# Optimization experiments

Measured on AMD Instinct MI355X. Metric: run time of the kernel, lower is better.

## Reference

```python
import jax, jax.numpy as jnp
import numpy as np

B, F, H, T = 2048, 128, 512, 96  # batch, n_features, hidden_size, output_length


def setup_inputs() -> dict:
    key = jax.random.key(0)
    ks = jax.random.split(key, 7)
    s_ih = 1.0 / np.sqrt(H)
    return {
        "hidden": jax.random.normal(ks[0], (B, H), dtype=jnp.float32),
        "w_ih": jax.random.uniform(ks[1], (3 * H, F), jnp.float32, -s_ih, s_ih),
        "w_hh": jax.random.uniform(ks[2], (3 * H, H), jnp.float32, -s_ih, s_ih),
        "b_ih": jax.random.uniform(ks[3], (3 * H,), jnp.float32, -s_ih, s_ih),
        "b_hh": jax.random.uniform(ks[4], (3 * H,), jnp.float32, -s_ih, s_ih),
        "fc_w": jax.random.uniform(ks[5], (F, H), jnp.float32, -s_ih, s_ih),
        "fc_b": jax.random.uniform(ks[6], (F,), jnp.float32, -s_ih, s_ih),
    }


def reference(hidden, w_ih, w_hh, b_ih, b_hh, fc_w, fc_b):
    x0 = jnp.zeros((hidden.shape[0], F), dtype=hidden.dtype)  # initial_input=None

    def step(carry, _):
        h, x = carry
        gi = x @ w_ih.T + b_ih            # [B, 3H]
        gh = h @ w_hh.T + b_hh            # [B, 3H]
        i_r, i_z, i_n = jnp.split(gi, 3, axis=-1)
        h_r, h_z, h_n = jnp.split(gh, 3, axis=-1)
        r = jax.nn.sigmoid(i_r + h_r)
        z = jax.nn.sigmoid(i_z + h_z)
        n = jnp.tanh(i_n + r * h_n)
        h_new = (1.0 - z) * n + z * h
        x_new = h_new @ fc_w.T + fc_b     # [B, F]
        return (h_new, x_new), x_new

    _, ys = jax.lax.scan(step, (hidden, x0), None, length=T)  # [T, B, F]
    out = jnp.transpose(ys, (1, 0, 2))     # [B, T, F]
    out = out[:, ::-1, :]                  # backwards=True: outputs.insert(0, ...)
    return out
```

## Files before the change

kernel.cpp:

```cpp
#include <hip/hip_runtime.h>
#include <hip/hip_bf16.h>

#define HH 512
#define FF 128
#define BB 2048
#define TT 96
#define NSTEP 96
#define NGATE 2048
#define NTOT 2176
#define GRP 16
#define CPB 32

typedef short short8 __attribute__((ext_vector_type(8)));
typedef float f32x4 __attribute__((ext_vector_type(4)));

__device__ __forceinline__ float sigmoidf_(float x) { return 1.f / (1.f + __expf(-x)); }
__device__ __forceinline__ float tanhf_(float x) {
    float e = __expf(-2.f * fabsf(x));
    float t = (1.f - e) / (1.f + e);
    return x < 0.f ? -t : t;
}

__device__ __forceinline__ size_t frag_off(int m, int k, int K) {
    return (size_t)((m >> 4) * (K >> 5) + (k >> 5)) * 1024
         + (size_t)(((k >> 3) & 3) * 256 + (m & 15) * 16 + (k & 7) * 2);
}

__device__ __forceinline__ short bf16bits(float f) {
    __hip_bfloat16 b = __float2bfloat16(f);
    return *(short*)&b;
}

__global__ __launch_bounds__(256) void build_weights(
    const float* __restrict__ w_ih, const float* __restrict__ w_hh,
    const float* __restrict__ b_ih, const float* __restrict__ b_hh,
    const float* __restrict__ fc_w, const float* __restrict__ fc_b,
    char* __restrict__ Wg, char* __restrict__ W0g, char* __restrict__ Wfc,
    float* __restrict__ bias, float* __restrict__ bias0)
{
    const int n = blockIdx.x;
    const int tid = threadIdx.x;
    __shared__ float wih_s[FF];
    const bool is_out = (n >= NGATE);
    int gate = 3, gidx = 0, f = 0;
    if (is_out) {
        f = n - NGATE;
    } else {
        int o = n >> 5;
        gate = (n >> 3) & 3;
        int j = o * 8 + (n & 7);
        gidx = (gate == 0) ? j : (gate == 1) ? (512 + j) : (1024 + j);
    }
    if (!is_out && gate != 3 && tid < FF) wih_s[tid] = w_ih[gidx * FF + tid];
    __syncthreads();

    for (int k = tid; k < HH; k += 256) {
        float w, w0;
        if (is_out) {
            w = fc_w[f * HH + k];
            w0 = 0.f;
        } else if (gate == 3) {
            w = w_hh[gidx * HH + k];
            w0 = w;
        } else {
            float comb = 0.f;
#pragma unroll 8
            for (int ff2 = 0; ff2 < FF; ++ff2) comb += wih_s[ff2] * fc_w[ff2 * HH + k];
            if (gate == 2) { w = comb; w0 = 0.f; }
            else { float whh = w_hh[gidx * HH + k]; w = whh + comb; w0 = whh; }
        }
        if (is_out) {
            *(short*)(Wfc + frag_off(f, k, HH)) = bf16bits(w);
        } else {
            *(short*)(Wg  + frag_off(n, k, HH)) = bf16bits(w);
            *(short*)(W0g + frag_off(n, k, HH)) = bf16bits(w0);
        }
    }
    if (tid == 0 && !is_out) {
        float b, b0;
        float cb = 0.f;
        if (gate != 3)
            for (int ff2 = 0; ff2 < FF; ++ff2) cb += fc_b[ff2] * w_ih[gidx * FF + ff2];
        if (gate <= 1)      { float s2 = b_ih[gidx] + b_hh[gidx]; b = s2 + cb; b0 = s2; }
        else if (gate == 2) { b = b_ih[gidx] + cb; b0 = b_ih[gidx]; }
        else                { b = b_hh[gidx]; b0 = b_hh[gidx]; }
        bias[n] = b; bias0[n] = b0;
    }
}

__global__ __launch_bounds__(256) void init_misc(
    const float* __restrict__ hidden, char* __restrict__ hfrag, int* __restrict__ cnt)
{
    int i = blockIdx.x * 256 + threadIdx.x;
    int row = i >> 6, k0 = (i & 63) << 3;
    short8 v;
#pragma unroll
    for (int t = 0; t < 8; ++t) v[t] = bf16bits(hidden[(size_t)row * HH + k0 + t]);
    *(short8*)(hfrag + frag_off(row, k0, HH)) = v;
    if (i < GRP * NSTEP * CPB) cnt[i] = 0;
}

__global__ __launch_bounds__(256, 2) void gru_persist(
    const char* __restrict__ Wg, const char* __restrict__ W0g, const char* __restrict__ Wfc,
    const float* __restrict__ bias, const float* __restrict__ bias0,
    const float* __restrict__ fc_b, const float* __restrict__ hidden,
    char* __restrict__ hfrag0, char* __restrict__ hfrag1,
    float* __restrict__ out, int* __restrict__ cnt)
{
    __shared__ __align__(16) short Bs[32768];
    __shared__ __align__(16) short hfr[2048];

    const int tid = threadIdx.x;
    const int lane = tid & 63, w = tid >> 6;
    const int l15 = lane & 15, quad = lane >> 4;
    const int g = blockIdx.x & 15, c = blockIdx.x >> 4;

    const char* aB0 = hfrag0 + (size_t)(g * 8 + w * 2) * 16384 + lane * 16;
    const char* aB1 = hfrag1 + (size_t)(g * 8 + w * 2) * 16384 + lane * 16;
    const char* bf  = Wfc + (size_t)(c & 7) * 16384 + lane * 16;
    const bool fcw = (w == (c >> 3));

    float bv[4];
#pragma unroll
    for (int ct = 0; ct < 4; ++ct) bv[ct] = bias[c * 64 + ct * 16 + l15];
    const float fcb = fc_b[(c & 7) * 16 + l15];

    float carry[2][2][4];
    if (l15 < 8) {
#pragma unroll
        for (int rt = 0; rt < 2; ++rt)
#pragma unroll
            for (int og = 0; og < 2; ++og)
#pragma unroll
                for (int rg = 0; rg < 4; ++rg)
                    carry[rt][og][rg] =
                        hidden[(size_t)(g * 128 + w * 32 + rt * 16 + quad * 4 + rg) * HH
                               + c * 16 + og * 8 + l15];
    }

    int* const fl = cnt + g * (NSTEP * CPB);

    {
        const char* wsrc = Wg + (size_t)c * 65536;
#pragma unroll
        for (int i = 0; i < 16; ++i) {
            int idx = i * 256 + tid;
            *(int4*)((char*)Bs + idx * 16) = *(const int4*)(wsrc + (size_t)idx * 16);
        }
    }
    __syncthreads();

    auto grp_wait = [&](int s) {
        if (w == 0) {
            if (lane < 32) {
                const int* fp = fl + s * CPB + lane;
                while (__hip_atomic_load(fp, __ATOMIC_RELAXED, __HIP_MEMORY_SCOPE_AGENT) == 0)
                    __builtin_amdgcn_s_sleep(1);
            }
            asm volatile("buffer_inv sc0\n\ts_waitcnt vmcnt(0)" ::: "memory");
        }
        __syncthreads();
        asm volatile("" ::: "memory");
    };

    auto epilogue = [&](f32x4 (&acc)[2][4], int s, char* hout) {
#pragma unroll
        for (int rt = 0; rt < 2; ++rt)
#pragma unroll
            for (int og = 0; og < 2; ++og)
#pragma unroll
                for (int rg = 0; rg < 4; ++rg) {
                    float arz = acc[rt][2 * og][rg], anh = acc[rt][2 * og + 1][rg];
                    float zsh = __shfl_xor(arz, 8, 64);
                    float hsh = __shfl_xor(anh, 8, 64);
                    if (l15 < 8) {
                        float r = sigmoidf_(arz);
                        float z = sigmoidf_(zsh);
                        float nv = tanhf_(anh + r * hsh);
                        float hn = (1.f - z) * nv + z * carry[rt][og][rg];
                        carry[rt][og][rg] = hn;
                        hfr[(w * 32 + rt * 16 + quad * 4 + rg) * 16 + og * 8 + l15] = bf16bits(hn);
                    }
                }
        __syncthreads();
        {
            int lrow = tid >> 1, half = tid & 1;
            size_t off = (size_t)((g * 8 + (lrow >> 4)) * 16 + (c >> 1)) * 1024
                       + (size_t)((((c << 1) + half) & 3) * 256 + (lrow & 15) * 16);
            *(int4*)(hout + off) = *(const int4*)&hfr[lrow * 16 + half * 8];
        }
        asm volatile("s_waitcnt vmcnt(0)" ::: "memory");
        __syncthreads();
        if (tid == 0)
            __hip_atomic_store(fl + s * CPB + c, 1, __ATOMIC_RELAXED, __HIP_MEMORY_SCOPE_AGENT);
    };

    {
        f32x4 acc[2][4];
#pragma unroll
        for (int ct = 0; ct < 4; ++ct) {
            float b0 = bias0[c * 64 + ct * 16 + l15];
            acc[0][ct] = (f32x4){b0, b0, b0, b0};
            acc[1][ct] = acc[0][ct];
        }
        const char* bb0 = W0g + (size_t)c * 65536 + lane * 16;
        short8 A[2][2]; short8 Bt[2][4];
#pragma unroll
        for (int p = 0; p < 2; ++p) {
#pragma unroll
            for (int rt = 0; rt < 2; ++rt)
                A[p][rt] = *(const short8*)(aB0 + rt * 16384 + p * 1024);
#pragma unroll
            for (int ct = 0; ct < 4; ++ct)
                Bt[p][ct] = *(const short8*)(bb0 + ct * 16384 + p * 1024);
        }
#pragma unroll
        for (int it = 0; it < 16; ++it) {
            const int sl = it & 1;
#pragma unroll
            for (int rt = 0; rt < 2; ++rt)
#pragma unroll
                for (int ct = 0; ct < 4; ++ct)
                    acc[rt][ct] = __builtin_amdgcn_mfma_f32_16x16x32_bf16(A[sl][rt], Bt[sl][ct], acc[rt][ct], 0, 0, 0);
            if (it + 2 < 16) {
#pragma unroll
                for (int rt = 0; rt < 2; ++rt)
                    A[sl][rt] = *(const short8*)(aB0 + rt * 16384 + (it + 2) * 1024);
#pragma unroll
                for (int ct = 0; ct < 4; ++ct)
                    Bt[sl][ct] = *(const short8*)(bb0 + ct * 16384 + (it + 2) * 1024);
            }
        }
        epilogue(acc, 0, hfrag1);
    }

    for (int s = 1; s < 96; ++s) {
        const char* ab = (s & 1) ? aB1 : aB0;
        char* hout = (s & 1) ? hfrag0 : hfrag1;
        const int tt = 96 - s;

        f32x4 acc[2][4];
#pragma unroll
        for (int ct = 0; ct < 4; ++ct) {
            acc[0][ct] = (f32x4){bv[ct], bv[ct], bv[ct], bv[ct]};
            acc[1][ct] = acc[0][ct];
        }
        f32x4 fca[2] = {{0.f,0.f,0.f,0.f},{0.f,0.f,0.f,0.f}};

        short8 Bt[2][4]; short8 Bf[4];
#pragma unroll
        for (int p = 0; p < 2; ++p)
#pragma unroll
            for (int ct = 0; ct < 4; ++ct)
                Bt[p][ct] = *(const short8*)((const char*)Bs + ct * 16384 + p * 1024 + lane * 16);
        if (fcw) {
#pragma unroll
            for (int p = 0; p < 4; ++p)
                Bf[p] = *(const short8*)(bf + p * 1024);
        }

        grp_wait(s - 1);

        short8 A[6][2];
#pragma unroll
        for (int p = 0; p < 6; ++p)
#pragma unroll
            for (int rt = 0; rt < 2; ++rt)
                A[p][rt] = *(const short8*)(ab + rt * 16384 + p * 1024);

#pragma unroll
        for (int it = 0; it < 16; ++it) {
            const int sa = it % 6, sb = it & 1, sf = it & 3;
#pragma unroll
            for (int rt = 0; rt < 2; ++rt)
#pragma unroll
                for (int ct = 0; ct < 4; ++ct)
                    acc[rt][ct] = __builtin_amdgcn_mfma_f32_16x16x32_bf16(A[sa][rt], Bt[sb][ct], acc[rt][ct], 0, 0, 0);
            if (fcw) {
                fca[0] = __builtin_amdgcn_mfma_f32_16x16x32_bf16(A[sa][0], Bf[sf], fca[0], 0, 0, 0);
                fca[1] = __builtin_amdgcn_mfma_f32_16x16x32_bf16(A[sa][1], Bf[sf], fca[1], 0, 0, 0);
            }
            if (it + 6 < 16) {
#pragma unroll
                for (int rt = 0; rt < 2; ++rt)
                    A[sa][rt] = *(const short8*)(ab + rt * 16384 + (it + 6) * 1024);
            }
            if (it + 2 < 16) {
#pragma unroll
                for (int ct = 0; ct < 4; ++ct)
                    Bt[sb][ct] = *(const short8*)((const char*)Bs + ct * 16384 + (it + 2) * 1024 + lane * 16);
            }
            if (fcw && it + 4 < 16) Bf[sf] = *(const short8*)(bf + (it + 4) * 1024);
        }

        if (fcw) {
#pragma unroll
            for (int rt = 0; rt < 2; ++rt)
#pragma unroll
                for (int rg = 0; rg < 4; ++rg)
                    out[(size_t)(g * 128 + w * 32 + rt * 16 + quad * 4 + rg) * (TT * FF)
                        + tt * FF + (c & 7) * 16 + l15] = fca[rt][rg] + fcb;
        }

        epilogue(acc, s, hout);
    }

    grp_wait(95);
    if (fcw) {
        f32x4 fca[2] = {{0.f,0.f,0.f,0.f},{0.f,0.f,0.f,0.f}};
        short8 A[4][2]; short8 Bf[4];
#pragma unroll
        for (int p = 0; p < 4; ++p) {
#pragma unroll
            for (int rt = 0; rt < 2; ++rt)
                A[p][rt] = *(const short8*)(aB0 + rt * 16384 + p * 1024);
            Bf[p] = *(const short8*)(bf + p * 1024);
        }
#pragma unroll
        for (int it = 0; it < 16; ++it) {
            const int sl = it & 3;
            fca[0] = __builtin_amdgcn_mfma_f32_16x16x32_bf16(A[sl][0], Bf[sl], fca[0], 0, 0, 0);
            fca[1] = __builtin_amdgcn_mfma_f32_16x16x32_bf16(A[sl][1], Bf[sl], fca[1], 0, 0, 0);
            if (it + 4 < 16) {
#pragma unroll
                for (int rt = 0; rt < 2; ++rt)
                    A[sl][rt] = *(const short8*)(aB0 + rt * 16384 + (it + 4) * 1024);
                Bf[sl] = *(const short8*)(bf + (it + 4) * 1024);
            }
        }
#pragma unroll
        for (int rt = 0; rt < 2; ++rt)
#pragma unroll
            for (int rg = 0; rg < 4; ++rg)
                out[(size_t)(g * 128 + w * 32 + rt * 16 + quad * 4 + rg) * (TT * FF)
                    + (c & 7) * 16 + l15] = fca[rt][rg] + fcb;
    }
}

extern "C" void kernel_launch(void* const* d_in, const int* in_sizes, int n_in,
                              void* d_out, int out_size, void* d_ws, size_t ws_size,
                              hipStream_t stream) {
    const float* hidden = (const float*)d_in[0];
    const float* w_ih   = (const float*)d_in[1];
    const float* w_hh   = (const float*)d_in[2];
    const float* b_ih   = (const float*)d_in[3];
    const float* b_hh   = (const float*)d_in[4];
    const float* fc_w   = (const float*)d_in[5];
    const float* fc_b   = (const float*)d_in[6];
    float* out = (float*)d_out;

    char* ws = (char*)d_ws;
    size_t off = 0;
    auto alloc = [&](size_t bytes) -> void* {
        void* p = ws + off;
        off += (bytes + 255) & ~(size_t)255;
        return p;
    };
    char* Wg   = (char*)alloc((size_t)NGATE * HH * 2);
    char* W0g  = (char*)alloc((size_t)NGATE * HH * 2);
    char* Wfc  = (char*)alloc((size_t)FF * HH * 2);
    float* bias  = (float*)alloc(NGATE * 4);
    float* bias0 = (float*)alloc(NGATE * 4);
    char* hfrag0 = (char*)alloc((size_t)BB * HH * 2);
    char* hfrag1 = (char*)alloc((size_t)BB * HH * 2);
    int* cnt = (int*)alloc((size_t)GRP * NSTEP * CPB * 4);

    build_weights<<<NTOT, 256, 0, stream>>>(w_ih, w_hh, b_ih, b_hh, fc_w, fc_b,
                                            Wg, W0g, Wfc, bias, bias0);
    init_misc<<<(BB * HH / 8 + 255) / 256, 256, 0, stream>>>(hidden, hfrag0, cnt);
    gru_persist<<<512, 256, 0, stream>>>(Wg, W0g, Wfc, bias, bias0, fc_b, hidden,
                                         hfrag0, hfrag1, out, cnt);
}
```

Measured before the change: 944.7 us.

## Transpose GRU MFMA tiling so gates land in one lane's accumulator

Interleaves the gate rows of the packed weight matrix (r, z, n_i, n_h per group of four) and swaps the MFMA operand roles so weights are the A operand and hidden state the B operand. Each lane's f32x4 accumulator then holds all four gate pre-activations for one hidden unit, which removes the cross-lane shuffles and the half-idle lanes in the epilogue. Each wave now covers 64 batch rows by 2 weight tiles instead of 32 rows by 4 tiles. The FC projection is spread across time steps and two waves so a different wave does it on different steps, and output and bias accesses are vectorized to f32x4. The risk is different LDS and global read patterns and changed register pressure.

After: 959.9 us. About the same (+1.6%).

```diff
diff --git a/kernel.cpp b/kernel.cpp
--- a/kernel.cpp
+++ b/kernel.cpp
@@ -46,9 +46,8 @@
     if (is_out) {
         f = n - NGATE;
     } else {
-        int o = n >> 5;
-        gate = (n >> 3) & 3;
-        int j = o * 8 + (n & 7);
+        int j = (n >> 4) * 4 + ((n >> 2) & 3);
+        gate = n & 3;
         gidx = (gate == 0) ? j : (gate == 1) ? (512 + j) : (1024 + j);
     }
     if (!is_out && gate != 3 && tid < FF) wih_s[tid] = w_ih[gidx * FF + tid];
@@ -115,28 +114,31 @@
     const int l15 = lane & 15, quad = lane >> 4;
     const int g = blockIdx.x & 15, c = blockIdx.x >> 4;
 
-    const char* aB0 = hfrag0 + (size_t)(g * 8 + w * 2) * 16384 + lane * 16;
-    const char* aB1 = hfrag1 + (size_t)(g * 8 + w * 2) * 16384 + lane * 16;
+    const int jtb = (w >> 1) * 2;
+    const int rbase = (w & 1) * 64;
+    const int cbase = jtb * 4;
+
+    const char* aB0 = hfrag0 + (size_t)(g * 8 + (w & 1) * 4) * 16384 + lane * 16;
+    const char* aB1 = hfrag1 + (size_t)(g * 8 + (w & 1) * 4) * 16384 + lane * 16;
     const char* bf  = Wfc + (size_t)(c & 7) * 16384 + lane * 16;
-    const bool fcw = (w == (c >> 3));
-
-    float bv[4];
-#pragma unroll
-    for (int ct = 0; ct < 4; ++ct) bv[ct] = bias[c * 64 + ct * 16 + l15];
-    const float fcb = fc_b[(c & 7) * 16 + l15];
-
-    float carry[2][2][4];
-    if (l15 < 8) {
-#pragma unroll
-        for (int rt = 0; rt < 2; ++rt)
-#pragma unroll
-            for (int og = 0; og < 2; ++og)
-#pragma unroll
-                for (int rg = 0; rg < 4; ++rg)
-                    carry[rt][og][rg] =
-                        hidden[(size_t)(g * 128 + w * 32 + rt * 16 + quad * 4 + rg) * HH
-                               + c * 16 + og * 8 + l15];
-    }
+    const char* wlds = (const char*)Bs + (size_t)jtb * 16384 + lane * 16;
+    const bool fcsel = (w == 0) || (w == 3);
+    const int fcq = c >> 3;
+
+    f32x4 bv4[2];
+#pragma unroll
+    for (int jtl = 0; jtl < 2; ++jtl)
+        bv4[jtl] = *(const f32x4*)&bias[(c * 4 + jtb + jtl) * 16 + quad * 4];
+    const f32x4 fcb4 = *(const f32x4*)&fc_b[(c & 7) * 16 + quad * 4];
+
+    float carry[2][4];
+#pragma unroll
+    for (int jtl = 0; jtl < 2; ++jtl)
+#pragma unroll
+        for (int bt = 0; bt < 4; ++bt)
+            carry[jtl][bt] =
+                hidden[(size_t)(g * 128 + rbase + bt * 16 + l15) * HH
+                       + c * 16 + cbase + jtl * 4 + quad];
 
     int* const fl = cnt + g * (NSTEP * CPB);
 
@@ -165,23 +167,17 @@
 
     auto epilogue = [&](f32x4 (&acc)[2][4], int s, char* hout) {
 #pragma unroll
-        for (int rt = 0; rt < 2; ++rt)
-#pragma unroll
-            for (int og = 0; og < 2; ++og)
-#pragma unroll
-                for (int rg = 0; rg < 4; ++rg) {
-                    float arz = acc[rt][2 * og][rg], anh = acc[rt][2 * og + 1][rg];
-                    float zsh = __shfl_xor(arz, 8, 64);
-                    float hsh = __shfl_xor(anh, 8, 64);
-                    if (l15 < 8) {
-                        float r = sigmoidf_(arz);
-                        float z = sigmoidf_(zsh);
-                        float nv = tanhf_(anh + r * hsh);
-                        float hn = (1.f - z) * nv + z * carry[rt][og][rg];
-                        carry[rt][og][rg] = hn;
-                        hfr[(w * 32 + rt * 16 + quad * 4 + rg) * 16 + og * 8 + l15] = bf16bits(hn);
-                    }
-                }
+        for (int jtl = 0; jtl < 2; ++jtl)
+#pragma unroll
+            for (int bt = 0; bt < 4; ++bt) {
+                f32x4 a = acc[jtl][bt];
+                float r  = sigmoidf_(a[0]);
+                float z  = sigmoidf_(a[1]);
+                float nv = tanhf_(a[2] + r * a[3]);
+                float hn = (1.f - z) * nv + z * carry[jtl][bt];
+                carry[jtl][bt] = hn;
+                hfr[(rbase + bt * 16 + l15) * 16 + cbase + jtl * 4 + quad] = bf16bits(hn);
+            }
         __syncthreads();
         {
             int lrow = tid >> 1, half = tid & 1;
@@ -198,37 +194,37 @@
     {
         f32x4 acc[2][4];
 #pragma unroll
-        for (int ct = 0; ct < 4; ++ct) {
-            float b0 = bias0[c * 64 + ct * 16 + l15];
-            acc[0][ct] = (f32x4){b0, b0, b0, b0};
-            acc[1][ct] = acc[0][ct];
-        }
-        const char* bb0 = W0g + (size_t)c * 65536 + lane * 16;
-        short8 A[2][2]; short8 Bt[2][4];
+        for (int jtl = 0; jtl < 2; ++jtl) {
+            f32x4 b0 = *(const f32x4*)&bias0[(c * 4 + jtb + jtl) * 16 + quad * 4];
+#pragma unroll
+            for (int bt = 0; bt < 4; ++bt) acc[jtl][bt] = b0;
+        }
+        const char* w0b = W0g + (size_t)(c * 4 + jtb) * 16384 + lane * 16;
+        short8 W0[2][2]; short8 Hb[2][4];
 #pragma unroll
         for (int p = 0; p < 2; ++p) {
 #pragma unroll
-            for (int rt = 0; rt < 2; ++rt)
-                A[p][rt] = *(const short8*)(aB0 + rt * 16384 + p * 1024);
-#pragma unroll
-            for (int ct = 0; ct < 4; ++ct)
-                Bt[p][ct] = *(const short8*)(bb0 + ct * 16384 + p * 1024);
+            for (int jtl = 0; jtl < 2; ++jtl)
+                W0[p][jtl] = *(const short8*)(w0b + (jtl * 16 + p) * 1024);
+#pragma unroll
+            for (int bt = 0; bt < 4; ++bt)
+                Hb[p][bt] = *(const short8*)(aB0 + bt * 16384 + p * 1024);
         }
 #pragma unroll
         for (int it = 0; it < 16; ++it) {
             const int sl = it & 1;
 #pragma unroll
-            for (int rt = 0; rt < 2; ++rt)
-#pragma unroll
-                for (int ct = 0; ct < 4; ++ct)
-                    acc[rt][ct] = __builtin_amdgcn_mfma_f32_16x16x32_bf16(A[sl][rt], Bt[sl][ct], acc[rt][ct], 0, 0, 0);
+            for (int jtl = 0; jtl < 2; ++jtl)
+#pragma unroll
+                for (int bt = 0; bt < 4; ++bt)
+                    acc[jtl][bt] = __builtin_amdgcn_mfma_f32_16x16x32_bf16(W0[sl][jtl], Hb[sl][bt], acc[jtl][bt], 0, 0, 0);
             if (it + 2 < 16) {
 #pragma unroll
-                for (int rt = 0; rt < 2; ++rt)
-                    A[sl][rt] = *(const short8*)(aB0 + rt * 16384 + (it + 2) * 1024);
-#pragma unroll
-                for (int ct = 0; ct < 4; ++ct)
-                    Bt[sl][ct] = *(const short8*)(bb0 + ct * 16384 + (it + 2) * 1024);
+                for (int jtl = 0; jtl < 2; ++jtl)
+                    W0[sl][jtl] = *(const short8*)(w0b + (jtl * 16 + it + 2) * 1024);
+#pragma unroll
+                for (int bt = 0; bt < 4; ++bt)
+                    Hb[sl][bt] = *(const short8*)(aB0 + bt * 16384 + (it + 2) * 1024);
             }
         }
         epilogue(acc, 0, hfrag1);
@@ -237,103 +233,104 @@
     for (int s = 1; s < 96; ++s) {
         const char* ab = (s & 1) ? aB1 : aB0;
         char* hout = (s & 1) ? hfrag0 : hfrag1;
-        const int tt = 96 - s;
+        const bool dofc = fcsel && ((s & 3) == fcq);
 
         f32x4 acc[2][4];
 #pragma unroll
-        for (int ct = 0; ct < 4; ++ct) {
-            acc[0][ct] = (f32x4){bv[ct], bv[ct], bv[ct], bv[ct]};
-            acc[1][ct] = acc[0][ct];
-        }
-        f32x4 fca[2] = {{0.f,0.f,0.f,0.f},{0.f,0.f,0.f,0.f}};
-
-        short8 Bt[2][4]; short8 Bf[4];
+        for (int jtl = 0; jtl < 2; ++jtl)
+#pragma unroll
+            for (int bt = 0; bt < 4; ++bt) acc[jtl][bt] = bv4[jtl];
+        f32x4 fca[4] = {{0.f,0.f,0.f,0.f},{0.f,0.f,0.f,0.f},{0.f,0.f,0.f,0.f},{0.f,0.f,0.f,0.f}};
+
+        short8 Wa[2][2]; short8 Wf[2];
 #pragma unroll
         for (int p = 0; p < 2; ++p)
 #pragma unroll
-            for (int ct = 0; ct < 4; ++ct)
-                Bt[p][ct] = *(const short8*)((const char*)Bs + ct * 16384 + p * 1024 + lane * 16);
-        if (fcw) {
-#pragma unroll
-            for (int p = 0; p < 4; ++p)
-                Bf[p] = *(const short8*)(bf + p * 1024);
+            for (int jtl = 0; jtl < 2; ++jtl)
+                Wa[p][jtl] = *(const short8*)(wlds + (size_t)(jtl * 16 + p) * 1024);
+        if (dofc) {
+            Wf[0] = *(const short8*)(bf);
+            Wf[1] = *(const short8*)(bf + 1024);
         }
 
         grp_wait(s - 1);
 
-        short8 A[6][2];
-#pragma unroll
-        for (int p = 0; p < 6; ++p)
-#pragma unroll
-            for (int rt = 0; rt < 2; ++rt)
-                A[p][rt] = *(const short8*)(ab + rt * 16384 + p * 1024);
+        short8 Hb[4][4];
+#pragma unroll
+        for (int p = 0; p < 4; ++p)
+#pragma unroll
+            for (int bt = 0; bt < 4; ++bt)
+                Hb[p][bt] = *(const short8*)(ab + bt * 16384 + p * 1024);
 
 #pragma unroll
         for (int it = 0; it < 16; ++it) {
-            const int sa = it % 6, sb = it & 1, sf = it & 3;
-#pragma unroll
-            for (int rt = 0; rt < 2; ++rt)
-#pragma unroll
-                for (int ct = 0; ct < 4; ++ct)
-                    acc[rt][ct] = __builtin_amdgcn_mfma_f32_16x16x32_bf16(A[sa][rt], Bt[sb][ct], acc[rt][ct], 0, 0, 0);
-            if (fcw) {
-                fca[0] = __builtin_amdgcn_mfma_f32_16x16x32_bf16(A[sa][0], Bf[sf], fca[0], 0, 0, 0);
-                fca[1] = __builtin_amdgcn_mfma_f32_16x16x32_bf16(A[sa][1], Bf[sf], fca[1], 0, 0, 0);
-            }
-            if (it + 6 < 16) {
-#pragma unroll
-                for (int rt = 0; rt < 2; ++rt)
-                    A[sa][rt] = *(const short8*)(ab + rt * 16384 + (it + 6) * 1024);
+            const int sa = it & 3, sw = it & 1;
+#pragma unroll
+            for (int jtl = 0; jtl < 2; ++jtl)
+#pragma unroll
+                for (int bt = 0; bt < 4; ++bt)
+                    acc[jtl][bt] = __builtin_amdgcn_mfma_f32_16x16x32_bf16(Wa[sw][jtl], Hb[sa][bt], acc[jtl][bt], 0, 0, 0);
+            if (dofc) {
+#pragma unroll
+                for (int bt = 0; bt < 4; ++bt)
+                    fca[bt] = __builtin_amdgcn_mfma_f32_16x16x32_bf16(Wf[sw], Hb[sa][bt], fca[bt], 0, 0, 0);
+            }
+            if (it + 4 < 16) {
+#pragma unroll
+                for (int bt = 0; bt < 4; ++bt)
+                    Hb[sa][bt] = *(const short8*)(ab + bt * 16384 + (it + 4) * 1024);
             }
             if (it + 2 < 16) {
 #pragma unroll
-                for (int ct = 0; ct < 4; ++ct)
-                    Bt[sb][ct] = *(const short8*)((const char*)Bs + ct * 16384 + (it + 2) * 1024 + lane * 16);
-            }
-            if (fcw && it + 4 < 16) Bf[sf] = *(const short8*)(bf + (it + 4) * 1024);
-        }
-
-        if (fcw) {
-#pragma unroll
-            for (int rt = 0; rt < 2; ++rt)
-#pragma unroll
-                for (int rg = 0; rg < 4; ++rg)
-                    out[(size_t)(g * 128 + w * 32 + rt * 16 + quad * 4 + rg) * (TT * FF)
-                        + tt * FF + (c & 7) * 16 + l15] = fca[rt][rg] + fcb;
+                for (int jtl = 0; jtl < 2; ++jtl)
+                    Wa[sw][jtl] = *(const short8*)(wlds + (size_t)(jtl * 16 + it + 2) * 1024);
+                if (dofc) Wf[sw] = *(const short8*)(bf + (size_t)(it + 2) * 1024);
+            }
+        }
+
+        if (dofc) {
+            const int tt = 96 - s;
+#pragma unroll
+            for (int bt = 0; bt < 4; ++bt) {
+                f32x4 v = fca[bt] + fcb4;
+                *(f32x4*)&out[(size_t)(g * 128 + rbase + bt * 16 + l15) * (TT * FF)
+                              + tt * FF + (c & 7) * 16 + quad * 4] = v;
+            }
         }
 
         epilogue(acc, s, hout);
     }
 
     grp_wait(95);
-    if (fcw) {
-        f32x4 fca[2] = {{0.f,0.f,0.f,0.f},{0.f,0.f,0.f,0.f}};
-        short8 A[4][2]; short8 Bf[4];
-#pragma unroll
-        for (int p = 0; p < 4; ++p) {
-#pragma unroll
-            for (int rt = 0; rt < 2; ++rt)
-                A[p][rt] = *(const short8*)(aB0 + rt * 16384 + p * 1024);
-            Bf[p] = *(const short8*)(bf + p * 1024);
+    if (fcsel && fcq == 0) {
+        f32x4 fca[4] = {{0.f,0.f,0.f,0.f},{0.f,0.f,0.f,0.f},{0.f,0.f,0.f,0.f},{0.f,0.f,0.f,0.f}};
+        short8 Wf[2]; short8 Hb[2][4];
+#pragma unroll
+        for (int p = 0; p < 2; ++p) {
+            Wf[p] = *(const short8*)(bf + (size_t)p * 1024);
+#pragma unroll
+            for (int bt = 0; bt < 4; ++bt)
+                Hb[p][bt] = *(const short8*)(aB0 + bt * 16384 + p * 1024);
         }
 #pragma unroll
         for (int it = 0; it < 16; ++it) {
-            const int sl = it & 3;
-            fca[0] = __builtin_amdgcn_mfma_f32_16x16x32_bf16(A[sl][0], Bf[sl], fca[0], 0, 0, 0);
-            fca[1] = __builtin_amdgcn_mfma_f32_16x16x32_bf16(A[sl][1], Bf[sl], fca[1], 0, 0, 0);
-            if (it + 4 < 16) {
-#pragma unroll
-                for (int rt = 0; rt < 2; ++rt)
-                    A[sl][rt] = *(const short8*)(aB0 + rt * 16384 + (it + 4) * 1024);
-                Bf[sl] = *(const short8*)(bf + (it + 4) * 1024);
-            }
-        }
-#pragma unroll
-        for (int rt = 0; rt < 2; ++rt)
-#pragma unroll
-            for (int rg = 0; rg < 4; ++rg)
-                out[(size_t)(g * 128 + w * 32 + rt * 16 + quad * 4 + rg) * (TT * FF)
-                    + (c & 7) * 16 + l15] = fca[rt][rg] + fcb;
+            const int sl = it & 1;
+#pragma unroll
+            for (int bt = 0; bt < 4; ++bt)
+                fca[bt] = __builtin_amdgcn_mfma_f32_16x16x32_bf16(Wf[sl], Hb[sl][bt], fca[bt], 0, 0, 0);
+            if (it + 2 < 16) {
+                Wf[sl] = *(const short8*)(bf + (size_t)(it + 2) * 1024);
+#pragma unroll
+                for (int bt = 0; bt < 4; ++bt)
+                    Hb[sl][bt] = *(const short8*)(aB0 + bt * 16384 + (it + 2) * 1024);
+            }
+        }
+#pragma unroll
+        for (int bt = 0; bt < 4; ++bt) {
+            f32x4 v = fca[bt] + fcb4;
+            *(f32x4*)&out[(size_t)(g * 128 + rbase + bt * 16 + l15) * (TT * FF)
+                          + (c & 7) * 16 + quad * 4] = v;
+        }
     }
 }
 
```
